# Kernel tuning notes

Hardware: AMD Instinct MI355X
Metric: run time of the kernel (lower is better)

Reference implementation:

```python
import jax, jax.numpy as jnp
import numpy as np

PC_RANGE = (-50.0, -50.0, -4.0, 50.0, 50.0, 4.0)
IMG_H, IMG_W = 256.0, 704.0
EPS = 1e-5


def _bilinear_sample(feat, u, v):
    # feat [H,W,C]; u,v [M] in [0,1]; matches F.grid_sample(align_corners=False, padding_mode='zeros')
    H, W, _ = feat.shape
    x = u * W - 0.5
    y = v * H - 0.5
    x0 = jnp.floor(x)
    y0 = jnp.floor(y)
    dx = (x - x0)[:, None]
    dy = (y - y0)[:, None]
    x0 = x0.astype(jnp.int32)
    y0 = y0.astype(jnp.int32)

    def g(xi, yi):
        inb = ((xi >= 0) & (xi < W) & (yi >= 0) & (yi < H)).astype(feat.dtype)[:, None]
        return feat[jnp.clip(yi, 0, H - 1), jnp.clip(xi, 0, W - 1)] * inb

    return (g(x0, y0) * (1 - dx) * (1 - dy) + g(x0 + 1, y0) * dx * (1 - dy)
            + g(x0, y0 + 1) * (1 - dx) * dy + g(x0 + 1, y0 + 1) * dx * dy)


def _conv1x1(t, w, b):
    return jnp.einsum('bchw,oc->bohw', t, w) + b[None, :, None, None]


def _inorm(t, eps=1e-5):
    # InstanceNorm2d (affine=False): normalize per (b, c) over spatial dims
    m = t.mean(axis=(2, 3), keepdims=True)
    var = t.var(axis=(2, 3), keepdims=True)
    return (t - m) * jax.lax.rsqrt(var + eps)


def _forward(feat, lidar2img, bev_pos, pe_w1, pe_b1, pe_w2, pe_b2, pe_w3, pe_b3,
             c1_w, c1_b, c2_w, c2_b, c3_w, c3_b):
    B, N, C, Hf, Wf = feat.shape
    _, P, Hb, Wb, _ = bev_pos.shape
    Q = Hb * Wb
    lo = jnp.asarray(PC_RANGE[:3], feat.dtype)
    hi = jnp.asarray(PC_RANGE[3:], feat.dtype)
    # 'b p h w d -> b (h w) p d', then scale normalized coords into pc_range
    ref01 = jnp.transpose(bev_pos, (0, 2, 3, 1, 4)).reshape(B, Q, P, 3)
    ref = ref01 * (hi - lo) + lo
    # project through per-camera lidar2img (homogeneous)
    pts = jnp.concatenate([ref, jnp.ones_like(ref[..., :1])], axis=-1)  # [B,Q,P,4]
    cam = jnp.einsum('bnij,bqpj->bnqpi', lidar2img, pts)                # [B,N,Q,P,4]
    homo = cam[..., 2]
    z = jnp.maximum(homo, EPS)
    u = cam[..., 0] / z / IMG_W
    v = cam[..., 1] / z / IMG_H
    valid = ((homo > EPS) & (u > 0.0) & (u < 1.0) & (v > 0.0) & (v < 1.0)).astype(feat.dtype)
    # bilinear gather per camera; feats to channel-last ('b n (g c) h w -> (b g) n h w c', G=1)
    fmap = jnp.transpose(feat, (0, 1, 3, 4, 2)).reshape(B * N, Hf, Wf, C)
    samp = jax.vmap(_bilinear_sample)(fmap, u.reshape(B * N, Q * P), v.reshape(B * N, Q * P))
    samp = samp.reshape(B, N, Q, P, C) * valid[..., None]
    samp = samp.sum(axis=1)  # sum over cameras -> [B,Q,P,C]
    # PositionalEncodingMap(3 -> 256 -> 256 -> 128) on normalized reference points
    pe = jax.nn.relu(ref01 @ pe_w1 + pe_b1)
    pe = jax.nn.relu(pe @ pe_w2 + pe_b2)
    pe = pe @ pe_w3 + pe_b3
    samp = samp + pe
    # 'b (h w) g p c -> b (p g c) h w' with g=1
    x = jnp.transpose(samp.reshape(B, Hb, Wb, P, C), (0, 3, 4, 1, 2)).reshape(B, P * C, Hb, Wb)
    gelu = lambda t: jax.nn.gelu(t, approximate=False)
    x = gelu(_inorm(_conv1x1(x, c1_w, c1_b)))
    x = gelu(_inorm(_conv1x1(x, c2_w, c2_b)))
    x = _conv1x1(x, c3_w, c3_b)
    return x


def setup_inputs() -> dict:
    key = jax.random.key(0)
    ks = jax.random.split(key, 16)
    B, N, C, Hf, Wf = 1, 6, 128, 32, 88
    P, Hb, Wb = 4, 160, 160
    E = 128
    MID = 256
    s = 0.02
    return {
        'feat': jax.random.normal(ks[0], (B, N, C, Hf, Wf), jnp.float32),
        'lidar2img': jax.random.normal(ks[1], (B, N, 4, 4), jnp.float32),
        'bev_pos': jax.random.uniform(ks[2], (B, P, Hb, Wb, 3), jnp.float32),
        'pe_w1': jax.random.normal(ks[3], (3, MID), jnp.float32) * s,
        'pe_b1': jnp.zeros((MID,), jnp.float32),
        'pe_w2': jax.random.normal(ks[4], (MID, MID), jnp.float32) * s,
        'pe_b2': jnp.zeros((MID,), jnp.float32),
        'pe_w3': jax.random.normal(ks[5], (MID, E), jnp.float32) * s,
        'pe_b3': jnp.zeros((E,), jnp.float32),
        'c1_w': jax.random.normal(ks[6], (4 * E, P * 128), jnp.float32) * s,
        'c1_b': jnp.zeros((4 * E,), jnp.float32),
        'c2_w': jax.random.normal(ks[7], (E, 4 * E), jnp.float32) * s,
        'c2_b': jnp.zeros((E,), jnp.float32),
        'c3_w': jax.random.normal(ks[8], (E, E), jnp.float32) * s,
        'c3_b': jnp.zeros((E,), jnp.float32),
    }


def reference(feat, lidar2img, bev_pos, pe_w1, pe_b1, pe_w2, pe_b2, pe_w3, pe_b3,
              c1_w, c1_b, c2_w, c2_b, c3_w, c3_b):
    return _forward(feat, lidar2img, bev_pos, pe_w1, pe_b1, pe_w2, pe_b2, pe_w3, pe_b3,
                    c1_w, c1_b, c2_w, c2_b, c3_w, c3_b)
```

## Files before the change

### kernel.cpp

```cpp
#include <hip/hip_runtime.h>
#include <cstdint>
#include <cstddef>

using frag8 = __attribute__((ext_vector_type(8))) short;
using f32x4 = __attribute__((ext_vector_type(4))) float;

__device__ __forceinline__ float b2f_bits(unsigned short u) {
    union { uint32_t u32; float f; } x; x.u32 = ((uint32_t)u) << 16; return x.f;
}
__device__ __forceinline__ float b2f_lo(uint32_t pk) {
    return __builtin_bit_cast(float, pk << 16);
}
__device__ __forceinline__ float b2f_hi(uint32_t pk) {
    return __builtin_bit_cast(float, pk & 0xffff0000u);
}
__device__ __forceinline__ unsigned short f2b(float f) {
    uint32_t u = __builtin_bit_cast(uint32_t, f);
    uint32_t r = (u + 0x7fffu + ((u >> 16) & 1u)) >> 16;
    return (unsigned short)r;
}

#define HF 32
#define WFEAT 88
#define NCAM 6
#define NPT 102400
#define BM 128
#define BN 128
#define BK 64

__global__ __launch_bounds__(256) void k_prep(const float* __restrict__ feat,
                                              const float* __restrict__ pw2,
                                              const float* __restrict__ pw3,
                                              const float* __restrict__ c1w,
                                              const float* __restrict__ c2w,
                                              const float* __restrict__ c3w,
                                              const float* __restrict__ l2i,
                                              const float* __restrict__ bev,
                                              unsigned short* __restrict__ featT,
                                              unsigned short* __restrict__ W2Tb,
                                              unsigned short* __restrict__ W3Tb,
                                              unsigned short* __restrict__ C1Wb,
                                              unsigned short* __restrict__ C2Wb,
                                              unsigned short* __restrict__ C3Wb,
                                              float* __restrict__ stats,
                                              int* __restrict__ poff,
                                              float4* __restrict__ pwts) {
    __shared__ unsigned short tile[64 * 132];
    int b = blockIdx.x, t = threadIdx.x;
    if (b < 2400) {
        int idx = b * 256 + t;
        int n = idx / NPT, pt = idx - n * NPT;
        int q = pt >> 2, p = pt & 3;
        int h = q / 160, w = q - h * 160;
        const float* bv = bev + ((p * 160 + h) * 160 + w) * 3;
        float rx = bv[0] * 100.f - 50.f;
        float ry = bv[1] * 100.f - 50.f;
        float rz = bv[2] * 8.f - 4.f;
        const float* M = l2i + n * 16;
        float c0   = M[0] * rx + M[1] * ry + M[2]  * rz + M[3];
        float c1v  = M[4] * rx + M[5] * ry + M[6]  * rz + M[7];
        float homo = M[8] * rx + M[9] * ry + M[10] * rz + M[11];
        float z = fmaxf(homo, 1e-5f);
        float u = c0 / z / 704.0f;
        float v = c1v / z / 256.0f;
        if (!(homo > 1e-5f && u > 0.f && u < 1.f && v > 0.f && v < 1.f)) {
            poff[idx] = -1;
            return;
        }
        float fx = u * (float)WFEAT - 0.5f;
        float fy = v * (float)HF - 0.5f;
        float fx0 = floorf(fx), fy0 = floorf(fy);
        float dx = fx - fx0, dy = fy - fy0;
        int x0 = (int)fx0, y0 = (int)fy0;
        float wxa = (x0 < 0) ? dx : 1.f - dx;
        float wxb = (x0 >= 0 && x0 < WFEAT - 1) ? dx : 0.f;
        float wya = (y0 < 0) ? dy : 1.f - dy;
        float wyb = (y0 >= 0 && y0 < HF - 1) ? dy : 0.f;
        int bx = max(x0, 0), by = max(y0, 0);
        poff[idx] = ((n * HF + by) * WFEAT + bx) << 7;
        pwts[idx] = make_float4(wxa * wya, wxb * wya, wxa * wyb, wxb * wyb);
        return;
    }
    b -= 2400;
    if (b < 264) {
        int n = b / 44;
        int s0 = (b - n * 44) * 64;
        #pragma unroll
        for (int i = 0; i < 32; ++i) {
            int e = i * 256 + t;
            int c = e >> 6, sl = e & 63;
            tile[sl * 132 + c] = f2b(feat[(size_t)(n * 128 + c) * 2816 + s0 + sl]);
        }
        __syncthreads();
        #pragma unroll
        for (int j = 0; j < 8; ++j) {
            int flat = j * 1024 + t * 4;
            int sl = flat >> 7, c = flat & 127;
            ushort4 v = *(const ushort4*)(tile + sl * 132 + c);
            *(ushort4*)(featT + (size_t)(n * 2816 + s0 + sl) * 128 + c) = v;
        }
        return;
    }
    b -= 264;
    if (b < 256) {
        int idx = b * 256 + t;
        int r = idx >> 8, c = idx & 255;
        W2Tb[c * 256 + r] = f2b(pw2[idx]);
        return;
    }
    b -= 256;
    if (b < 128) {
        int idx = b * 256 + t;
        int r = idx >> 7, c = idx & 127;
        W3Tb[c * 256 + r] = f2b(pw3[idx]);
        return;
    }
    b -= 128;
    if (b < 1024) { int idx = b * 256 + t; C1Wb[idx] = f2b(c1w[idx]); return; }
    b -= 1024;
    if (b < 256)  { int idx = b * 256 + t; C2Wb[idx] = f2b(c2w[idx]); return; }
    b -= 256;
    if (b < 64)   { int idx = b * 256 + t; C3Wb[idx] = f2b(c3w[idx]); return; }
    #pragma unroll
    for (int j = 0; j < 10; ++j) stats[t * 10 + j] = 0.f;
}

__global__ __launch_bounds__(256) void k_sample2(const unsigned short* __restrict__ featT,
                                                 const int* __restrict__ poff,
                                                 const float4* __restrict__ pwts,
                                                 unsigned short* __restrict__ samp) {
    int pt = blockIdx.x * 4 + (threadIdx.x >> 6);
    int lane = threadIdx.x & 63;
    int c2 = lane * 2;
    int offs[NCAM];
    float4 ww[NCAM];
    #pragma unroll
    for (int n = 0; n < NCAM; ++n) offs[n] = poff[n * NPT + pt];
    #pragma unroll
    for (int n = 0; n < NCAM; ++n) ww[n] = pwts[n * NPT + pt];
    float acc0 = 0.f, acc1 = 0.f;
    #pragma unroll
    for (int n = 0; n < NCAM; ++n) {
        if (offs[n] >= 0) {
            const unsigned short* base = featT + offs[n] + c2;
            uint32_t p00 = *(const uint32_t*)(base);
            uint32_t p01 = *(const uint32_t*)(base + 128);
            uint32_t p10 = *(const uint32_t*)(base + WFEAT * 128);
            uint32_t p11 = *(const uint32_t*)(base + WFEAT * 128 + 128);
            float4 w = ww[n];
            acc0 += w.x * b2f_lo(p00) + w.y * b2f_lo(p01) + w.z * b2f_lo(p10) + w.w * b2f_lo(p11);
            acc1 += w.x * b2f_hi(p00) + w.y * b2f_hi(p01) + w.z * b2f_hi(p10) + w.w * b2f_hi(p11);
        }
    }
    uint32_t outpk = (uint32_t)f2b(acc0) | ((uint32_t)f2b(acc1) << 16);
    *(uint32_t*)(samp + (size_t)pt * 128 + c2) = outpk;
}

__device__ __forceinline__ void stage_tile(const unsigned short* __restrict__ g, int ld,
                                           unsigned short* lds, int wave, int lane) {
    #pragma unroll
    for (int j = 0; j < 4; ++j) {
        int idx = wave * 256 + j * 64 + lane;
        int r = idx >> 3;
        int cs = idx & 7;
        int cl = cs ^ (r & 7);
        __builtin_amdgcn_global_load_lds(
            (const __attribute__((address_space(1))) void*)(g + (size_t)r * ld + cl * 8),
            (__attribute__((address_space(3))) void*)(lds + wave * 2048 + j * 512),
            16, 0, 0);
    }
}

__device__ __forceinline__ frag8 frag_read(const unsigned short* lds, int row, int chunk) {
    return *(const frag8*)(lds + row * 64 + ((chunk ^ (row & 7)) << 3));
}

__device__ __forceinline__ void mma_tile(const unsigned short* As, const unsigned short* Bs,
                                         int wm, int wn, int lane, f32x4 (&acc)[4][4]) {
    int lm = lane & 15, lq = lane >> 4;
    #pragma unroll
    for (int kk = 0; kk < 2; ++kk) {
        frag8 a[4], b[4];
        #pragma unroll
        for (int t = 0; t < 4; ++t) a[t] = frag_read(As, wm * 64 + t * 16 + lm, kk * 4 + lq);
        #pragma unroll
        for (int t = 0; t < 4; ++t) b[t] = frag_read(Bs, wn * 64 + t * 16 + lm, kk * 4 + lq);
        #pragma unroll
        for (int tm = 0; tm < 4; ++tm)
            #pragma unroll
            for (int tn = 0; tn < 4; ++tn)
                acc[tm][tn] = __builtin_amdgcn_mfma_f32_16x16x32_bf16(a[tm], b[tn], acc[tm][tn], 0, 0, 0);
    }
}

__global__ __launch_bounds__(256) void k_pe12(const float* __restrict__ bev,
                                              const float* __restrict__ pw1,
                                              const float* __restrict__ pb1,
                                              const unsigned short* __restrict__ Bt,
                                              const float* __restrict__ bias,
                                              unsigned short* __restrict__ H2) {
    __shared__ unsigned short As[BM * BK], Bs[BN * BK];
    __shared__ __align__(16) float wls[4 * 256];
    __shared__ float bevs[3 * 128];
    int t = threadIdx.x, lane = t & 63, wave = t >> 6;
    int wm = wave >> 1, wn = wave & 1;
    int m0 = blockIdx.x * BM, n0 = blockIdx.y * BN;
    {
        int i = t * 4;
        int j = i >> 8, c = i & 255;
        float4 v = (j < 3) ? *(const float4*)(pw1 + j * 256 + c)
                           : *(const float4*)(pb1 + c);
        *(float4*)(wls + i) = v;
    }
    if (t < 128) {
        int m = m0 + t;
        int q = m >> 2, p = m & 3;
        int h = q / 160, w = q - h * 160;
        const float* bv = bev + ((size_t)((p * 160 + h) * 160 + w)) * 3;
        bevs[t] = bv[0]; bevs[128 + t] = bv[1]; bevs[256 + t] = bv[2];
    }
    __syncthreads();
    int r = t & 127;
    int c0 = (t >> 7) * 4;
    float x = bevs[r], y = bevs[128 + r], z = bevs[256 + r];
    f32x4 acc[4][4] = {};
    for (int kt = 0; kt < 4; ++kt) {
        stage_tile(Bt + (size_t)n0 * 256 + kt * BK, 256, Bs, wave, lane);
        #pragma unroll
        for (int j = 0; j < 4; ++j) {
            int cl = c0 + j;
            const float* wp = wls + kt * 64 + cl * 8;
            float4 a0l = *(const float4*)(wp),       a0h = *(const float4*)(wp + 4);
            float4 a1l = *(const float4*)(wp + 256), a1h = *(const float4*)(wp + 260);
            float4 a2l = *(const float4*)(wp + 512), a2h = *(const float4*)(wp + 516);
            float4 bbl = *(const float4*)(wp + 768), bbh = *(const float4*)(wp + 772);
            uint32_t q0 = (uint32_t)f2b(fmaxf(x * a0l.x + y * a1l.x + z * a2l.x + bbl.x, 0.f))
                        | ((uint32_t)f2b(fmaxf(x * a0l.y + y * a1l.y + z * a2l.y + bbl.y, 0.f)) << 16);
            uint32_t q1 = (uint32_t)f2b(fmaxf(x * a0l.z + y * a1l.z + z * a2l.z + bbl.z, 0.f))
                        | ((uint32_t)f2b(fmaxf(x * a0l.w + y * a1l.w + z * a2l.w + bbl.w, 0.f)) << 16);
            uint32_t q2 = (uint32_t)f2b(fmaxf(x * a0h.x + y * a1h.x + z * a2h.x + bbh.x, 0.f))
                        | ((uint32_t)f2b(fmaxf(x * a0h.y + y * a1h.y + z * a2h.y + bbh.y, 0.f)) << 16);
            uint32_t q3 = (uint32_t)f2b(fmaxf(x * a0h.z + y * a1h.z + z * a2h.z + bbh.z, 0.f))
                        | ((uint32_t)f2b(fmaxf(x * a0h.w + y * a1h.w + z * a2h.w + bbh.w, 0.f)) << 16);
            *(uint4*)(As + r * 64 + ((cl ^ (r & 7)) << 3)) = make_uint4(q0, q1, q2, q3);
        }
        __syncthreads();
        mma_tile(As, Bs, wm, wn, lane, acc);
        __syncthreads();
    }
    int lm = lane & 15, lq = lane >> 4;
    #pragma unroll
    for (int tn = 0; tn < 4; ++tn) {
        int n = n0 + wn * 64 + tn * 16 + lm;
        float bn = bias[n];
        #pragma unroll
        for (int tm = 0; tm < 4; ++tm) {
            int mb = m0 + wm * 64 + tm * 16 + lq * 4;
            #pragma unroll
            for (int rr = 0; rr < 4; ++rr)
                H2[(size_t)(mb + rr) * 256 + n] = f2b(fmaxf(acc[tm][tn][rr] + bn, 0.f));
        }
    }
}

__global__ __launch_bounds__(256) void k_gemm_pe3(const unsigned short* __restrict__ A,
                                                  const unsigned short* __restrict__ Bt,
                                                  const float* __restrict__ bias,
                                                  const unsigned short* __restrict__ samp,
                                                  unsigned short* __restrict__ X) {
    __shared__ unsigned short As[BM * BK], Bs[BN * BK];
    int lane = threadIdx.x & 63, wave = threadIdx.x >> 6;
    int wm = wave >> 1, wn = wave & 1;
    int m0 = blockIdx.x * BM;
    f32x4 acc[4][4] = {};
    for (int kt = 0; kt < 4; ++kt) {
        stage_tile(A + (size_t)m0 * 256 + kt * BK, 256, As, wave, lane);
        stage_tile(Bt + (size_t)kt * BK, 256, Bs, wave, lane);
        __syncthreads();
        mma_tile(As, Bs, wm, wn, lane, acc);
        __syncthreads();
    }
    int lm = lane & 15, lq = lane >> 4;
    #pragma unroll
    for (int tn = 0; tn < 4; ++tn) {
        int n = wn * 64 + tn * 16 + lm;
        float bn = bias[n];
        #pragma unroll
        for (int tm = 0; tm < 4; ++tm) {
            int mb = m0 + wm * 64 + tm * 16 + lq * 4;
            #pragma unroll
            for (int rr = 0; rr < 4; ++rr) {
                size_t off = (size_t)(mb + rr) * 128 + n;
                X[off] = f2b(acc[tm][tn][rr] + bn + b2f_bits(samp[off]));
            }
        }
    }
}

template <int K, bool STATS>
__global__ __launch_bounds__(256) void k_gemm_conv(const unsigned short* __restrict__ A,
                                                   const unsigned short* __restrict__ Bt,
                                                   const float* __restrict__ bias,
                                                   unsigned short* __restrict__ Y, int ldY,
                                                   float* __restrict__ st, int C) {
    __shared__ unsigned short As[BM * BK], Bs[BN * BK];
    int lane = threadIdx.x & 63, wave = threadIdx.x >> 6;
    int wm = wave >> 1, wn = wave & 1;
    int m0 = blockIdx.x * BM, n0 = blockIdx.y * BN;
    f32x4 acc[4][4] = {};
    for (int kt = 0; kt < K / BK; ++kt) {
        stage_tile(A + (size_t)m0 * K + kt * BK, K, As, wave, lane);
        stage_tile(Bt + (size_t)n0 * K + kt * BK, K, Bs, wave, lane);
        __syncthreads();
        mma_tile(As, Bs, wm, wn, lane, acc);
        __syncthreads();
    }
    int lm = lane & 15, lq = lane >> 4;
    #pragma unroll
    for (int tn = 0; tn < 4; ++tn) {
        int n = n0 + wn * 64 + tn * 16 + lm;
        float bn = bias[n];
        float s1 = 0.f, s2 = 0.f;
        #pragma unroll
        for (int tm = 0; tm < 4; ++tm) {
            int mb = m0 + wm * 64 + tm * 16 + lq * 4;
            #pragma unroll
            for (int rr = 0; rr < 4; ++rr) {
                float v = acc[tm][tn][rr] + bn;
                Y[(size_t)(mb + rr) * ldY + n] = f2b(v);
                if (STATS) { s1 += v; s2 += v * v; }
            }
        }
        if (STATS) {
            s1 += __shfl_xor(s1, 16); s1 += __shfl_xor(s1, 32);
            s2 += __shfl_xor(s2, 16); s2 += __shfl_xor(s2, 32);
            if (lq == 0) { atomicAdd(&st[n], s1); atomicAdd(&st[C + n], s2); }
        }
    }
}

__global__ __launch_bounds__(256) void k_gemm_conv3(const unsigned short* __restrict__ A,
                                                    const unsigned short* __restrict__ Bt,
                                                    const float* __restrict__ bias,
                                                    float* __restrict__ out) {
    __shared__ unsigned short As[BM * BK], Bs[BN * BK];
    int lane = threadIdx.x & 63, wave = threadIdx.x >> 6;
    int wm = wave >> 1, wn = wave & 1;
    int m0 = blockIdx.x * BM;
    f32x4 acc[4][4] = {};
    for (int kt = 0; kt < 2; ++kt) {
        stage_tile(A + (size_t)m0 * 128 + kt * BK, 128, As, wave, lane);
        stage_tile(Bt + (size_t)kt * BK, 128, Bs, wave, lane);
        __syncthreads();
        mma_tile(As, Bs, wm, wn, lane, acc);
        __syncthreads();
    }
    int lm = lane & 15, lq = lane >> 4;
    #pragma unroll
    for (int tn = 0; tn < 4; ++tn) {
        int n = wn * 64 + tn * 16 + lm;
        float bn = bias[n];
        #pragma unroll
        for (int tm = 0; tm < 4; ++tm) {
            int mb = m0 + wm * 64 + tm * 16 + lq * 4;
            float4 pk;
            pk.x = acc[tm][tn][0] + bn;
            pk.y = acc[tm][tn][1] + bn;
            pk.z = acc[tm][tn][2] + bn;
            pk.w = acc[tm][tn][3] + bn;
            *(float4*)(out + (size_t)n * 25600 + mb) = pk;
        }
    }
}

__global__ void k_normgelu8f(const unsigned short* __restrict__ Y, const float* __restrict__ st,
                             unsigned short* __restrict__ X2, int Cmask, int C, float inv_n,
                             int total8) {
    int i8 = blockIdx.x * 256 + threadIdx.x;
    if (i8 >= total8) return;
    int e0 = i8 * 8;
    int c = e0 & Cmask;
    uint4 y = *(const uint4*)(Y + e0);
    float4 s1a = *(const float4*)(st + c);
    float4 s1b = *(const float4*)(st + c + 4);
    float4 s2a = *(const float4*)(st + C + c);
    float4 s2b = *(const float4*)(st + C + c + 4);
    float mu[8] = { s1a.x * inv_n, s1a.y * inv_n, s1a.z * inv_n, s1a.w * inv_n,
                    s1b.x * inv_n, s1b.y * inv_n, s1b.z * inv_n, s1b.w * inv_n };
    float sq[8] = { s2a.x, s2a.y, s2a.z, s2a.w, s2b.x, s2b.y, s2b.z, s2b.w };
    float rs[8];
    #pragma unroll
    for (int j = 0; j < 8; ++j) rs[j] = rsqrtf(sq[j] * inv_n - mu[j] * mu[j] + 1e-5f);
    const float is2 = 0.70710678118654752f;
    unsigned int yw[4] = {y.x, y.y, y.z, y.w};
    unsigned int ow[4];
    #pragma unroll
    for (int j = 0; j < 4; ++j) {
        float v0 = (b2f_bits((unsigned short)(yw[j] & 0xffffu)) - mu[j * 2]) * rs[j * 2];
        float v1 = (b2f_bits((unsigned short)(yw[j] >> 16)) - mu[j * 2 + 1]) * rs[j * 2 + 1];
        float g0 = 0.5f * v0 * (1.f + erff(v0 * is2));
        float g1 = 0.5f * v1 * (1.f + erff(v1 * is2));
        ow[j] = (uint32_t)f2b(g0) | ((uint32_t)f2b(g1) << 16);
    }
    *(uint4*)(X2 + e0) = make_uint4(ow[0], ow[1], ow[2], ow[3]);
}

extern "C" void kernel_launch(void* const* d_in, const int* in_sizes, int n_in,
                              void* d_out, int out_size, void* d_ws, size_t ws_size,
                              hipStream_t stream) {
    (void)in_sizes; (void)n_in; (void)out_size; (void)ws_size;
    const float* feat = (const float*)d_in[0];
    const float* l2i  = (const float*)d_in[1];
    const float* bev  = (const float*)d_in[2];
    const float* pw1  = (const float*)d_in[3];
    const float* pb1  = (const float*)d_in[4];
    const float* pw2  = (const float*)d_in[5];
    const float* pb2  = (const float*)d_in[6];
    const float* pw3  = (const float*)d_in[7];
    const float* pb3  = (const float*)d_in[8];
    const float* c1w  = (const float*)d_in[9];
    const float* c1b  = (const float*)d_in[10];
    const float* c2w  = (const float*)d_in[11];
    const float* c2b  = (const float*)d_in[12];
    const float* c3w  = (const float*)d_in[13];
    const float* c3b  = (const float*)d_in[14];
    float* outp = (float*)d_out;
    char* ws = (char*)d_ws;

    unsigned short* featT = (unsigned short*)(ws + 0);
    unsigned short* W2Tb  = (unsigned short*)(ws + 4348416);
    unsigned short* W3Tb  = (unsigned short*)(ws + 4479488);
    unsigned short* C1Wb  = (unsigned short*)(ws + 4545024);
    unsigned short* C2Wb  = (unsigned short*)(ws + 5069312);
    unsigned short* C3Wb  = (unsigned short*)(ws + 5200384);
    float* stats          = (float*)(ws + 5233152);
    int*    poff          = (int*)(ws + 5247488);
    float4* pwts          = (float4*)(ws + 7705088);
    char* BUF1 = ws + 17535488;
    char* BUF2 = ws + 69964288;
    char* BUF3 = ws + 122393088;

    float* st512 = stats;
    float* st128 = stats + 2048;

    unsigned short* H2   = (unsigned short*)BUF2;
    unsigned short* samp = (unsigned short*)BUF3;
    unsigned short* X    = (unsigned short*)BUF1;
    unsigned short* Y1   = (unsigned short*)BUF2;
    unsigned short* X2   = (unsigned short*)BUF3;
    unsigned short* Y2   = (unsigned short*)BUF1;
    unsigned short* X3   = (unsigned short*)(BUF1 + 6553600);

    k_prep<<<4393, 256, 0, stream>>>(feat, pw2, pw3, c1w, c2w, c3w, l2i, bev,
                                     featT, W2Tb, W3Tb, C1Wb, C2Wb, C3Wb, stats,
                                     poff, pwts);

    k_sample2<<<25600, 256, 0, stream>>>(featT, poff, pwts, samp);

    k_pe12<<<dim3(800, 2), 256, 0, stream>>>(bev, pw1, pb1, W2Tb, pb2, H2);
    k_gemm_pe3<<<dim3(800, 1), 256, 0, stream>>>(H2, W3Tb, pb3, samp, X);

    k_gemm_conv<512, true><<<dim3(200, 4), 256, 0, stream>>>(X, C1Wb, c1b, Y1, 512, st512, 512);
    k_normgelu8f<<<6400, 256, 0, stream>>>(Y1, st512, X2, 511, 512, 1.f / 25600.f, 1638400);

    k_gemm_conv<512, true><<<dim3(200, 1), 256, 0, stream>>>(X2, C2Wb, c2b, Y2, 128, st128, 128);
    k_normgelu8f<<<1600, 256, 0, stream>>>(Y2, st128, X3, 127, 128, 1.f / 25600.f, 409600);

    k_gemm_conv3<<<dim3(200, 1), 256, 0, stream>>>(X3, C3Wb, c3b, outp);
}
```

Before: 278.5 us.

## Fuse instance-norm+GELU into following GEMM prologues and double-buffer LDS tiles

Removes the two standalone norm+GELU kernels and applies normalization and GELU while loading A tiles inside the conv2 and conv3 GEMMs, so the normalized intermediates are never written to or read back from global memory. All GEMM kernels switch to double-buffered LDS so the next tile is staged while MFMAs run on the current one. The on-the-fly first PE layer in k_pe12 is overlapped the same way and now packs to bf16 with v_cvt_pk_bf16_f32. In exchange, LDS per block doubles, which may lower occupancy, and the erf work is repeated per block (conv2/conv3 have a single N tile, so nothing is recomputed).

```diff
diff --git a/kernel.cpp b/kernel.cpp
--- a/kernel.cpp
+++ b/kernel.cpp
@@ -18,6 +18,11 @@
     uint32_t u = __builtin_bit_cast(uint32_t, f);
     uint32_t r = (u + 0x7fffu + ((u >> 16) & 1u)) >> 16;
     return (unsigned short)r;
+}
+__device__ __forceinline__ uint32_t cvtpk_bf16(float lo, float hi) {
+    uint32_t r;
+    asm("v_cvt_pk_bf16_f32 %0, %1, %2" : "=v"(r) : "v"(lo), "v"(hi));
+    return r;
 }
 
 #define HF 32
@@ -193,13 +198,59 @@
     }
 }
 
+template <int KT>
+__device__ __forceinline__ void gemm_loop_db(const unsigned short* __restrict__ A, int ldA,
+                                             const unsigned short* __restrict__ B, int ldB,
+                                             unsigned short (*As)[BM * BK],
+                                             unsigned short (*Bs)[BN * BK],
+                                             int wave, int lane, int wm, int wn,
+                                             f32x4 (&acc)[4][4]) {
+    stage_tile(A, ldA, As[0], wave, lane);
+    stage_tile(B, ldB, Bs[0], wave, lane);
+    __syncthreads();
+    #pragma unroll
+    for (int kt = 0; kt < KT; ++kt) {
+        int cur = kt & 1, nxt = cur ^ 1;
+        if (kt + 1 < KT) {
+            stage_tile(A + (kt + 1) * BK, ldA, As[nxt], wave, lane);
+            stage_tile(B + (kt + 1) * BK, ldB, Bs[nxt], wave, lane);
+        }
+        mma_tile(As[cur], Bs[cur], wm, wn, lane, acc);
+        __syncthreads();
+    }
+}
+
+__device__ __forceinline__ void build_h1(const float* __restrict__ wls, float x, float y, float z,
+                                         int r, int c0, int kt, unsigned short* __restrict__ As) {
+    #pragma unroll
+    for (int j = 0; j < 4; ++j) {
+        int cl = c0 + j;
+        const float* wp = wls + kt * 64 + cl * 8;
+        float4 a0l = *(const float4*)(wp),       a0h = *(const float4*)(wp + 4);
+        float4 a1l = *(const float4*)(wp + 256), a1h = *(const float4*)(wp + 260);
+        float4 a2l = *(const float4*)(wp + 512), a2h = *(const float4*)(wp + 516);
+        float4 bbl = *(const float4*)(wp + 768), bbh = *(const float4*)(wp + 772);
+        float v0 = fmaxf(x * a0l.x + y * a1l.x + z * a2l.x + bbl.x, 0.f);
+        float v1 = fmaxf(x * a0l.y + y * a1l.y + z * a2l.y + bbl.y, 0.f);
+        float v2 = fmaxf(x * a0l.z + y * a1l.z + z * a2l.z + bbl.z, 0.f);
+        float v3 = fmaxf(x * a0l.w + y * a1l.w + z * a2l.w + bbl.w, 0.f);
+        float v4 = fmaxf(x * a0h.x + y * a1h.x + z * a2h.x + bbh.x, 0.f);
+        float v5 = fmaxf(x * a0h.y + y * a1h.y + z * a2h.y + bbh.y, 0.f);
+        float v6 = fmaxf(x * a0h.z + y * a1h.z + z * a2h.z + bbh.z, 0.f);
+        float v7 = fmaxf(x * a0h.w + y * a1h.w + z * a2h.w + bbh.w, 0.f);
+        uint32_t q0 = cvtpk_bf16(v0, v1), q1 = cvtpk_bf16(v2, v3);
+        uint32_t q2 = cvtpk_bf16(v4, v5), q3 = cvtpk_bf16(v6, v7);
+        *(uint4*)(As + r * 64 + ((cl ^ (r & 7)) << 3)) = make_uint4(q0, q1, q2, q3);
+    }
+}
+
 __global__ __launch_bounds__(256) void k_pe12(const float* __restrict__ bev,
                                               const float* __restrict__ pw1,
                                               const float* __restrict__ pb1,
                                               const unsigned short* __restrict__ Bt,
                                               const float* __restrict__ bias,
                                               unsigned short* __restrict__ H2) {
-    __shared__ unsigned short As[BM * BK], Bs[BN * BK];
+    __shared__ unsigned short As[2][BM * BK], Bs[2][BN * BK];
     __shared__ __align__(16) float wls[4 * 256];
     __shared__ float bevs[3 * 128];
     int t = threadIdx.x, lane = t & 63, wave = t >> 6;
@@ -224,28 +275,17 @@
     int c0 = (t >> 7) * 4;
     float x = bevs[r], y = bevs[128 + r], z = bevs[256 + r];
     f32x4 acc[4][4] = {};
+    stage_tile(Bt + (size_t)n0 * 256, 256, Bs[0], wave, lane);
+    build_h1(wls, x, y, z, r, c0, 0, As[0]);
+    __syncthreads();
+    #pragma unroll
     for (int kt = 0; kt < 4; ++kt) {
-        stage_tile(Bt + (size_t)n0 * 256 + kt * BK, 256, Bs, wave, lane);
-        #pragma unroll
-        for (int j = 0; j < 4; ++j) {
-            int cl = c0 + j;
-            const float* wp = wls + kt * 64 + cl * 8;
-            float4 a0l = *(const float4*)(wp),       a0h = *(const float4*)(wp + 4);
-            float4 a1l = *(const float4*)(wp + 256), a1h = *(const float4*)(wp + 260);
-            float4 a2l = *(const float4*)(wp + 512), a2h = *(const float4*)(wp + 516);
-            float4 bbl = *(const float4*)(wp + 768), bbh = *(const float4*)(wp + 772);
-            uint32_t q0 = (uint32_t)f2b(fmaxf(x * a0l.x + y * a1l.x + z * a2l.x + bbl.x, 0.f))
-                        | ((uint32_t)f2b(fmaxf(x * a0l.y + y * a1l.y + z * a2l.y + bbl.y, 0.f)) << 16);
-            uint32_t q1 = (uint32_t)f2b(fmaxf(x * a0l.z + y * a1l.z + z * a2l.z + bbl.z, 0.f))
-                        | ((uint32_t)f2b(fmaxf(x * a0l.w + y * a1l.w + z * a2l.w + bbl.w, 0.f)) << 16);
-            uint32_t q2 = (uint32_t)f2b(fmaxf(x * a0h.x + y * a1h.x + z * a2h.x + bbh.x, 0.f))
-                        | ((uint32_t)f2b(fmaxf(x * a0h.y + y * a1h.y + z * a2h.y + bbh.y, 0.f)) << 16);
-            uint32_t q3 = (uint32_t)f2b(fmaxf(x * a0h.z + y * a1h.z + z * a2h.z + bbh.z, 0.f))
-                        | ((uint32_t)f2b(fmaxf(x * a0h.w + y * a1h.w + z * a2h.w + bbh.w, 0.f)) << 16);
-            *(uint4*)(As + r * 64 + ((cl ^ (r & 7)) << 3)) = make_uint4(q0, q1, q2, q3);
-        }
-        __syncthreads();
-        mma_tile(As, Bs, wm, wn, lane, acc);
+        int cur = kt & 1, nxt = cur ^ 1;
+        if (kt < 3)
+            stage_tile(Bt + (size_t)n0 * 256 + (kt + 1) * BK, 256, Bs[nxt], wave, lane);
+        mma_tile(As[cur], Bs[cur], wm, wn, lane, acc);
+        if (kt < 3)
+            build_h1(wls, x, y, z, r, c0, kt + 1, As[nxt]);
         __syncthreads();
     }
     int lm = lane & 15, lq = lane >> 4;
@@ -268,18 +308,12 @@
                                                   const float* __restrict__ bias,
                                                   const unsigned short* __restrict__ samp,
                                                   unsigned short* __restrict__ X) {
-    __shared__ unsigned short As[BM * BK], Bs[BN * BK];
+    __shared__ unsigned short As[2][BM * BK], Bs[2][BN * BK];
     int lane = threadIdx.x & 63, wave = threadIdx.x >> 6;
     int wm = wave >> 1, wn = wave & 1;
     int m0 = blockIdx.x * BM;
     f32x4 acc[4][4] = {};
-    for (int kt = 0; kt < 4; ++kt) {
-        stage_tile(A + (size_t)m0 * 256 + kt * BK, 256, As, wave, lane);
-        stage_tile(Bt + (size_t)kt * BK, 256, Bs, wave, lane);
-        __syncthreads();
-        mma_tile(As, Bs, wm, wn, lane, acc);
-        __syncthreads();
-    }
+    gemm_loop_db<4>(A + (size_t)m0 * 256, 256, Bt, 256, As, Bs, wave, lane, wm, wn, acc);
     int lm = lane & 15, lq = lane >> 4;
     #pragma unroll
     for (int tn = 0; tn < 4; ++tn) {
@@ -303,18 +337,13 @@
                                                    const float* __restrict__ bias,
                                                    unsigned short* __restrict__ Y, int ldY,
                                                    float* __restrict__ st, int C) {
-    __shared__ unsigned short As[BM * BK], Bs[BN * BK];
+    __shared__ unsigned short As[2][BM * BK], Bs[2][BN * BK];
     int lane = threadIdx.x & 63, wave = threadIdx.x >> 6;
     int wm = wave >> 1, wn = wave & 1;
     int m0 = blockIdx.x * BM, n0 = blockIdx.y * BN;
     f32x4 acc[4][4] = {};
-    for (int kt = 0; kt < K / BK; ++kt) {
-        stage_tile(A + (size_t)m0 * K + kt * BK, K, As, wave, lane);
-        stage_tile(Bt + (size_t)n0 * K + kt * BK, K, Bs, wave, lane);
-        __syncthreads();
-        mma_tile(As, Bs, wm, wn, lane, acc);
-        __syncthreads();
-    }
+    gemm_loop_db<K / BK>(A + (size_t)m0 * K, K, Bt + (size_t)n0 * K, K,
+                         As, Bs, wave, lane, wm, wn, acc);
     int lm = lane & 15, lq = lane >> 4;
     #pragma unroll
     for (int tn = 0; tn < 4; ++tn) {
@@ -339,20 +368,125 @@
     }
 }
 
-__global__ __launch_bounds__(256) void k_gemm_conv3(const unsigned short* __restrict__ A,
-                                                    const unsigned short* __restrict__ Bt,
-                                                    const float* __restrict__ bias,
-                                                    float* __restrict__ out) {
-    __shared__ unsigned short As[BM * BK], Bs[BN * BK];
-    int lane = threadIdx.x & 63, wave = threadIdx.x >> 6;
+__device__ __forceinline__ void ng_load(const unsigned short* __restrict__ Ain, int ldA,
+                                        int m0, int k0, uint4 (&yv)[4], int wave, int lane) {
+    #pragma unroll
+    for (int j = 0; j < 4; ++j) {
+        int idx = wave * 256 + j * 64 + lane;
+        int r = idx >> 3, cs = idx & 7;
+        int cl = cs ^ (r & 7);
+        yv[j] = *(const uint4*)(Ain + (size_t)(m0 + r) * ldA + k0 + cl * 8);
+    }
+}
+
+__device__ __forceinline__ void ng_write(const uint4 (&yv)[4], const float* __restrict__ st,
+                                         int C, float inv_n, int k0,
+                                         unsigned short* __restrict__ lds, int wave, int lane) {
+    const float is2 = 0.70710678118654752f;
+    #pragma unroll
+    for (int j = 0; j < 4; ++j) {
+        int idx = wave * 256 + j * 64 + lane;
+        int r = idx >> 3, cs = idx & 7;
+        int cl = cs ^ (r & 7);
+        int k = k0 + cl * 8;
+        float4 s1a = *(const float4*)(st + k);
+        float4 s1b = *(const float4*)(st + k + 4);
+        float4 s2a = *(const float4*)(st + C + k);
+        float4 s2b = *(const float4*)(st + C + k + 4);
+        float s1[8] = {s1a.x, s1a.y, s1a.z, s1a.w, s1b.x, s1b.y, s1b.z, s1b.w};
+        float s2[8] = {s2a.x, s2a.y, s2a.z, s2a.w, s2b.x, s2b.y, s2b.z, s2b.w};
+        uint32_t yw[4] = {yv[j].x, yv[j].y, yv[j].z, yv[j].w};
+        uint32_t ow[4];
+        #pragma unroll
+        for (int i = 0; i < 4; ++i) {
+            float mu0 = s1[2 * i] * inv_n,     mu1 = s1[2 * i + 1] * inv_n;
+            float rs0 = rsqrtf(s2[2 * i] * inv_n - mu0 * mu0 + 1e-5f);
+            float rs1 = rsqrtf(s2[2 * i + 1] * inv_n - mu1 * mu1 + 1e-5f);
+            float v0 = (b2f_lo(yw[i]) - mu0) * rs0;
+            float v1 = (b2f_hi(yw[i]) - mu1) * rs1;
+            float g0 = 0.5f * v0 * (1.f + erff(v0 * is2));
+            float g1 = 0.5f * v1 * (1.f + erff(v1 * is2));
+            ow[i] = (uint32_t)f2b(g0) | ((uint32_t)f2b(g1) << 16);
+        }
+        *(uint4*)(lds + idx * 8) = make_uint4(ow[0], ow[1], ow[2], ow[3]);
+    }
+}
+
+__global__ __launch_bounds__(256) void k_gemm_conv2f(const unsigned short* __restrict__ Y1,
+                                                     const float* __restrict__ stIn,
+                                                     const unsigned short* __restrict__ Bt,
+                                                     const float* __restrict__ bias,
+                                                     unsigned short* __restrict__ Y2,
+                                                     float* __restrict__ stOut) {
+    __shared__ unsigned short As[2][BM * BK], Bs[2][BN * BK];
+    int t = threadIdx.x, lane = t & 63, wave = t >> 6;
     int wm = wave >> 1, wn = wave & 1;
     int m0 = blockIdx.x * BM;
+    const float inv_n = 1.f / 25600.f;
     f32x4 acc[4][4] = {};
+    uint4 yv[4];
+    ng_load(Y1, 512, m0, 0, yv, wave, lane);
+    stage_tile(Bt, 512, Bs[0], wave, lane);
+    ng_write(yv, stIn, 512, inv_n, 0, As[0], wave, lane);
+    __syncthreads();
+    #pragma unroll
+    for (int kt = 0; kt < 8; ++kt) {
+        int cur = kt & 1, nxt = cur ^ 1;
+        if (kt < 7) {
+            stage_tile(Bt + (kt + 1) * BK, 512, Bs[nxt], wave, lane);
+            ng_load(Y1, 512, m0, (kt + 1) * BK, yv, wave, lane);
+        }
+        mma_tile(As[cur], Bs[cur], wm, wn, lane, acc);
+        if (kt < 7) ng_write(yv, stIn, 512, inv_n, (kt + 1) * BK, As[nxt], wave, lane);
+        __syncthreads();
+    }
+    int lm = lane & 15, lq = lane >> 4;
+    #pragma unroll
+    for (int tn = 0; tn < 4; ++tn) {
+        int n = wn * 64 + tn * 16 + lm;
+        float bn = bias[n];
+        float s1 = 0.f, s2 = 0.f;
+        #pragma unroll
+        for (int tm = 0; tm < 4; ++tm) {
+            int mb = m0 + wm * 64 + tm * 16 + lq * 4;
+            #pragma unroll
+            for (int rr = 0; rr < 4; ++rr) {
+                float v = acc[tm][tn][rr] + bn;
+                Y2[(size_t)(mb + rr) * 128 + n] = f2b(v);
+                s1 += v; s2 += v * v;
+            }
+        }
+        s1 += __shfl_xor(s1, 16); s1 += __shfl_xor(s1, 32);
+        s2 += __shfl_xor(s2, 16); s2 += __shfl_xor(s2, 32);
+        if (lq == 0) { atomicAdd(&stOut[n], s1); atomicAdd(&stOut[128 + n], s2); }
+    }
+}
+
+__global__ __launch_bounds__(256) void k_gemm_conv3f(const unsigned short* __restrict__ Y2,
+                                                     const float* __restrict__ stIn,
+                                                     const unsigned short* __restrict__ Bt,
+                                                     const float* __restrict__ bias,
+                                                     float* __restrict__ out) {
+    __shared__ unsigned short As[2][BM * BK], Bs[2][BN * BK];
+    int t = threadIdx.x, lane = t & 63, wave = t >> 6;
+    int wm = wave >> 1, wn = wave & 1;
+    int m0 = blockIdx.x * BM;
+    const float inv_n = 1.f / 25600.f;
+    f32x4 acc[4][4] = {};
+    uint4 yv[4];
+    ng_load(Y2, 128, m0, 0, yv, wave, lane);
+    stage_tile(Bt, 128, Bs[0], wave, lane);
+    ng_write(yv, stIn, 128, inv_n, 0, As[0], wave, lane);
+    __syncthreads();
+    #pragma unroll
     for (int kt = 0; kt < 2; ++kt) {
-        stage_tile(A + (size_t)m0 * 128 + kt * BK, 128, As, wave, lane);
-        stage_tile(Bt + (size_t)kt * BK, 128, Bs, wave, lane);
-        __syncthreads();
-        mma_tile(As, Bs, wm, wn, lane, acc);
+        int cur = kt & 1, nxt = cur ^ 1;
+        if (kt < 1) {
+            stage_tile(Bt + (kt + 1) * BK, 128, Bs[nxt], wave, lane);
+            ng_load(Y2, 128, m0, (kt + 1) * BK, yv, wave, lane);
+        }
+        mma_tile(As[cur], Bs[cur], wm, wn, lane, acc);
+        if (kt < 1) ng_write(yv, stIn, 128, inv_n, (kt + 1) * BK, As[nxt], wave, lane);
         __syncthreads();
     }
     int lm = lane & 15, lq = lane >> 4;
@@ -371,38 +505,6 @@
             *(float4*)(out + (size_t)n * 25600 + mb) = pk;
         }
     }
-}
-
-__global__ void k_normgelu8f(const unsigned short* __restrict__ Y, const float* __restrict__ st,
-                             unsigned short* __restrict__ X2, int Cmask, int C, float inv_n,
-                             int total8) {
-    int i8 = blockIdx.x * 256 + threadIdx.x;
-    if (i8 >= total8) return;
-    int e0 = i8 * 8;
-    int c = e0 & Cmask;
-    uint4 y = *(const uint4*)(Y + e0);
-    float4 s1a = *(const float4*)(st + c);
-    float4 s1b = *(const float4*)(st + c + 4);
-    float4 s2a = *(const float4*)(st + C + c);
-    float4 s2b = *(const float4*)(st + C + c + 4);
-    float mu[8] = { s1a.x * inv_n, s1a.y * inv_n, s1a.z * inv_n, s1a.w * inv_n,
-                    s1b.x * inv_n, s1b.y * inv_n, s1b.z * inv_n, s1b.w * inv_n };
-    float sq[8] = { s2a.x, s2a.y, s2a.z, s2a.w, s2b.x, s2b.y, s2b.z, s2b.w };
-    float rs[8];
-    #pragma unroll
-    for (int j = 0; j < 8; ++j) rs[j] = rsqrtf(sq[j] * inv_n - mu[j] * mu[j] + 1e-5f);
-    const float is2 = 0.70710678118654752f;
-    unsigned int yw[4] = {y.x, y.y, y.z, y.w};
-    unsigned int ow[4];
-    #pragma unroll
-    for (int j = 0; j < 4; ++j) {
-        float v0 = (b2f_bits((unsigned short)(yw[j] & 0xffffu)) - mu[j * 2]) * rs[j * 2];
-        float v1 = (b2f_bits((unsigned short)(yw[j] >> 16)) - mu[j * 2 + 1]) * rs[j * 2 + 1];
-        float g0 = 0.5f * v0 * (1.f + erff(v0 * is2));
-        float g1 = 0.5f * v1 * (1.f + erff(v1 * is2));
-        ow[j] = (uint32_t)f2b(g0) | ((uint32_t)f2b(g1) << 16);
-    }
-    *(uint4*)(X2 + e0) = make_uint4(ow[0], ow[1], ow[2], ow[3]);
 }
 
 extern "C" void kernel_launch(void* const* d_in, const int* in_sizes, int n_in,
@@ -447,9 +549,7 @@
     unsigned short* samp = (unsigned short*)BUF3;
     unsigned short* X    = (unsigned short*)BUF1;
     unsigned short* Y1   = (unsigned short*)BUF2;
-    unsigned short* X2   = (unsigned short*)BUF3;
     unsigned short* Y2   = (unsigned short*)BUF1;
-    unsigned short* X3   = (unsigned short*)(BUF1 + 6553600);
 
     k_prep<<<4393, 256, 0, stream>>>(feat, pw2, pw3, c1w, c2w, c3w, l2i, bev,
                                      featT, W2Tb, W3Tb, C1Wb, C2Wb, C3Wb, stats,
@@ -461,10 +561,8 @@
     k_gemm_pe3<<<dim3(800, 1), 256, 0, stream>>>(H2, W3Tb, pb3, samp, X);
 
     k_gemm_conv<512, true><<<dim3(200, 4), 256, 0, stream>>>(X, C1Wb, c1b, Y1, 512, st512, 512);
-    k_normgelu8f<<<6400, 256, 0, stream>>>(Y1, st512, X2, 511, 512, 1.f / 25600.f, 1638400);
-
-    k_gemm_conv<512, true><<<dim3(200, 1), 256, 0, stream>>>(X2, C2Wb, c2b, Y2, 128, st128, 128);
-    k_normgelu8f<<<1600, 256, 0, stream>>>(Y2, st128, X3, 127, 128, 1.f / 25600.f, 409600);
-
-    k_gemm_conv3<<<dim3(200, 1), 256, 0, stream>>>(X3, C3Wb, c3b, outp);
-}
+
+    k_gemm_conv2f<<<dim3(200, 1), 256, 0, stream>>>(Y1, st512, C2Wb, c2b, Y2, st128);
+
+    k_gemm_conv3f<<<dim3(200, 1), 256, 0, stream>>>(Y2, st128, C3Wb, c3b, outp);
+}
```

Result: slower. 306.6 us (+10.1%).

## Fuse positional-encoding MLP layers into one kernel and double-buffer conv GEMMs

Applied to the files above, without the earlier changes.

Merges the pe layer1/2 kernel and the pe3 GEMM into a single kernel. Each block computes the full 256-wide hidden layer in registers, keeps H2 in shared memory, and runs the third layer with W3 fragments loaded straight from global. This removes the H2 global round trip and one launch, and stops layer 1 being recomputed for two N-tiles. The conv GEMMs get a double-buffered shared-memory K loop that overlaps staging of the next tile with MFMA. A hardware packed bf16 convert replaces the manual rounding for H1. The costs are higher register pressure (a 4x8 accumulator array), 64KB of shared memory per block that may limit occupancy, and uncached global reads of W3 per wave.

```diff
diff --git a/kernel.cpp b/kernel.cpp
--- a/kernel.cpp
+++ b/kernel.cpp
@@ -18,6 +18,11 @@
     uint32_t u = __builtin_bit_cast(uint32_t, f);
     uint32_t r = (u + 0x7fffu + ((u >> 16) & 1u)) >> 16;
     return (unsigned short)r;
+}
+__device__ __forceinline__ uint32_t cvtpk_bf16(float lo, float hi) {
+    uint32_t r;
+    asm("v_cvt_pk_bf16_f32 %0, %1, %2" : "=v"(r) : "v"(lo), "v"(hi));
+    return r;
 }
 
 #define HF 32
@@ -193,18 +198,71 @@
     }
 }
 
-__global__ __launch_bounds__(256) void k_pe12(const float* __restrict__ bev,
-                                              const float* __restrict__ pw1,
-                                              const float* __restrict__ pb1,
-                                              const unsigned short* __restrict__ Bt,
-                                              const float* __restrict__ bias,
-                                              unsigned short* __restrict__ H2) {
-    __shared__ unsigned short As[BM * BK], Bs[BN * BK];
-    __shared__ __align__(16) float wls[4 * 256];
-    __shared__ float bevs[3 * 128];
+template <int KT>
+__device__ __forceinline__ void gemm_loop_db(const unsigned short* __restrict__ A, int ldA,
+                                             const unsigned short* __restrict__ B, int ldB,
+                                             unsigned short (*As)[BM * BK],
+                                             unsigned short (*Bs)[BN * BK],
+                                             int wave, int lane, int wm, int wn,
+                                             f32x4 (&acc)[4][4]) {
+    stage_tile(A, ldA, As[0], wave, lane);
+    stage_tile(B, ldB, Bs[0], wave, lane);
+    __syncthreads();
+    #pragma unroll
+    for (int kt = 0; kt < KT; ++kt) {
+        int cur = kt & 1, nxt = cur ^ 1;
+        if (kt + 1 < KT) {
+            stage_tile(A + (kt + 1) * BK, ldA, As[nxt], wave, lane);
+            stage_tile(B + (kt + 1) * BK, ldB, Bs[nxt], wave, lane);
+        }
+        mma_tile(As[cur], Bs[cur], wm, wn, lane, acc);
+        __syncthreads();
+    }
+}
+
+__device__ __forceinline__ void build_h1(const float* __restrict__ wls, float x, float y, float z,
+                                         int r, int c0, int kt, unsigned short* __restrict__ As) {
+    #pragma unroll
+    for (int j = 0; j < 4; ++j) {
+        int cl = c0 + j;
+        const float* wp = wls + kt * 64 + cl * 8;
+        float4 a0l = *(const float4*)(wp),       a0h = *(const float4*)(wp + 4);
+        float4 a1l = *(const float4*)(wp + 256), a1h = *(const float4*)(wp + 260);
+        float4 a2l = *(const float4*)(wp + 512), a2h = *(const float4*)(wp + 516);
+        float4 bbl = *(const float4*)(wp + 768), bbh = *(const float4*)(wp + 772);
+        float v0 = fmaxf(x * a0l.x + y * a1l.x + z * a2l.x + bbl.x, 0.f);
+        float v1 = fmaxf(x * a0l.y + y * a1l.y + z * a2l.y + bbl.y, 0.f);
+        float v2 = fmaxf(x * a0l.z + y * a1l.z + z * a2l.z + bbl.z, 0.f);
+        float v3 = fmaxf(x * a0l.w + y * a1l.w + z * a2l.w + bbl.w, 0.f);
+        float v4 = fmaxf(x * a0h.x + y * a1h.x + z * a2h.x + bbh.x, 0.f);
+        float v5 = fmaxf(x * a0h.y + y * a1h.y + z * a2h.y + bbh.y, 0.f);
+        float v6 = fmaxf(x * a0h.z + y * a1h.z + z * a2h.z + bbh.z, 0.f);
+        float v7 = fmaxf(x * a0h.w + y * a1h.w + z * a2h.w + bbh.w, 0.f);
+        uint32_t q0 = cvtpk_bf16(v0, v1), q1 = cvtpk_bf16(v2, v3);
+        uint32_t q2 = cvtpk_bf16(v4, v5), q3 = cvtpk_bf16(v6, v7);
+        *(uint4*)(As + r * 64 + ((cl ^ (r & 7)) << 3)) = make_uint4(q0, q1, q2, q3);
+    }
+}
+
+__global__ __launch_bounds__(256) void k_pe123(const float* __restrict__ bev,
+                                               const float* __restrict__ pw1,
+                                               const float* __restrict__ pb1,
+                                               const unsigned short* __restrict__ W2t,
+                                               const float* __restrict__ pb2,
+                                               const unsigned short* __restrict__ W3t,
+                                               const float* __restrict__ pb3,
+                                               const unsigned short* __restrict__ samp,
+                                               unsigned short* __restrict__ X) {
+    __shared__ __align__(16) char smem[65536];
+    unsigned short* As  = (unsigned short*)smem;
+    unsigned short* Bs  = (unsigned short*)(smem + 16384);
+    float* wls  = (float*)(smem + 49152);
+    float* bevs = (float*)(smem + 53248);
+    unsigned short* H2s = (unsigned short*)smem;
+
     int t = threadIdx.x, lane = t & 63, wave = t >> 6;
     int wm = wave >> 1, wn = wave & 1;
-    int m0 = blockIdx.x * BM, n0 = blockIdx.y * BN;
+    int m0 = blockIdx.x * BM;
     {
         int i = t * 4;
         int j = i >> 8, c = i & 255;
@@ -223,75 +281,84 @@
     int r = t & 127;
     int c0 = (t >> 7) * 4;
     float x = bevs[r], y = bevs[128 + r], z = bevs[256 + r];
-    f32x4 acc[4][4] = {};
+    int lm = lane & 15, lq = lane >> 4;
+
+    f32x4 acc[4][8] = {};
     for (int kt = 0; kt < 4; ++kt) {
-        stage_tile(Bt + (size_t)n0 * 256 + kt * BK, 256, Bs, wave, lane);
-        #pragma unroll
-        for (int j = 0; j < 4; ++j) {
-            int cl = c0 + j;
-            const float* wp = wls + kt * 64 + cl * 8;
-            float4 a0l = *(const float4*)(wp),       a0h = *(const float4*)(wp + 4);
-            float4 a1l = *(const float4*)(wp + 256), a1h = *(const float4*)(wp + 260);
-            float4 a2l = *(const float4*)(wp + 512), a2h = *(const float4*)(wp + 516);
-            float4 bbl = *(const float4*)(wp + 768), bbh = *(const float4*)(wp + 772);
-            uint32_t q0 = (uint32_t)f2b(fmaxf(x * a0l.x + y * a1l.x + z * a2l.x + bbl.x, 0.f))
-                        | ((uint32_t)f2b(fmaxf(x * a0l.y + y * a1l.y + z * a2l.y + bbl.y, 0.f)) << 16);
-            uint32_t q1 = (uint32_t)f2b(fmaxf(x * a0l.z + y * a1l.z + z * a2l.z + bbl.z, 0.f))
-                        | ((uint32_t)f2b(fmaxf(x * a0l.w + y * a1l.w + z * a2l.w + bbl.w, 0.f)) << 16);
-            uint32_t q2 = (uint32_t)f2b(fmaxf(x * a0h.x + y * a1h.x + z * a2h.x + bbh.x, 0.f))
-                        | ((uint32_t)f2b(fmaxf(x * a0h.y + y * a1h.y + z * a2h.y + bbh.y, 0.f)) << 16);
-            uint32_t q3 = (uint32_t)f2b(fmaxf(x * a0h.z + y * a1h.z + z * a2h.z + bbh.z, 0.f))
-                        | ((uint32_t)f2b(fmaxf(x * a0h.w + y * a1h.w + z * a2h.w + bbh.w, 0.f)) << 16);
-            *(uint4*)(As + r * 64 + ((cl ^ (r & 7)) << 3)) = make_uint4(q0, q1, q2, q3);
-        }
+        stage_tile(W2t + kt * BK, 256, Bs, wave, lane);
+        stage_tile(W2t + 128 * 256 + kt * BK, 256, Bs + 8192, wave, lane);
+        build_h1(wls, x, y, z, r, c0, kt, As);
         __syncthreads();
-        mma_tile(As, Bs, wm, wn, lane, acc);
+        #pragma unroll
+        for (int kk = 0; kk < 2; ++kk) {
+            int ch = kk * 4 + lq;
+            frag8 a[4], b[8];
+            #pragma unroll
+            for (int tt = 0; tt < 4; ++tt) a[tt] = frag_read(As, wm * 64 + tt * 16 + lm, ch);
+            #pragma unroll
+            for (int tn = 0; tn < 8; ++tn) {
+                int brow = (tn < 4 ? wn * 64 + tn * 16 : 128 + wn * 64 + (tn - 4) * 16) + lm;
+                b[tn] = frag_read(Bs, brow, ch);
+            }
+            #pragma unroll
+            for (int tm = 0; tm < 4; ++tm)
+                #pragma unroll
+                for (int tn = 0; tn < 8; ++tn)
+                    acc[tm][tn] = __builtin_amdgcn_mfma_f32_16x16x32_bf16(a[tm], b[tn], acc[tm][tn], 0, 0, 0);
+        }
         __syncthreads();
     }
-    int lm = lane & 15, lq = lane >> 4;
+
+    #pragma unroll
+    for (int tn = 0; tn < 8; ++tn) {
+        int n = (tn < 4 ? wn * 64 + tn * 16 : 128 + wn * 64 + (tn - 4) * 16) + lm;
+        float bn = pb2[n];
+        int kt2 = n >> 6, chs = (n >> 3) & 7, e = n & 7;
+        #pragma unroll
+        for (int tm = 0; tm < 4; ++tm) {
+            int rb = wm * 64 + tm * 16 + lq * 4;
+            #pragma unroll
+            for (int rr = 0; rr < 4; ++rr) {
+                int row = rb + rr;
+                H2s[kt2 * 8192 + row * 64 + ((chs ^ (row & 7)) << 3) + e] =
+                    f2b(fmaxf(acc[tm][tn][rr] + bn, 0.f));
+            }
+        }
+    }
+    __syncthreads();
+
+    f32x4 acc2[4][4] = {};
+    #pragma unroll
+    for (int kt = 0; kt < 4; ++kt) {
+        #pragma unroll
+        for (int kk = 0; kk < 2; ++kk) {
+            int ch = kk * 4 + lq;
+            frag8 a[4], b[4];
+            #pragma unroll
+            for (int tt = 0; tt < 4; ++tt)
+                a[tt] = frag_read(H2s + kt * 8192, wm * 64 + tt * 16 + lm, ch);
+            #pragma unroll
+            for (int tn = 0; tn < 4; ++tn)
+                b[tn] = *(const frag8*)(W3t + (size_t)(wn * 64 + tn * 16 + lm) * 256 + kt * 64 + ch * 8);
+            #pragma unroll
+            for (int tm = 0; tm < 4; ++tm)
+                #pragma unroll
+                for (int tn = 0; tn < 4; ++tn)
+                    acc2[tm][tn] = __builtin_amdgcn_mfma_f32_16x16x32_bf16(a[tm], b[tn], acc2[tm][tn], 0, 0, 0);
+        }
+    }
+
     #pragma unroll
     for (int tn = 0; tn < 4; ++tn) {
-        int n = n0 + wn * 64 + tn * 16 + lm;
-        float bn = bias[n];
+        int n = wn * 64 + tn * 16 + lm;
+        float bn = pb3[n];
         #pragma unroll
         for (int tm = 0; tm < 4; ++tm) {
             int mb = m0 + wm * 64 + tm * 16 + lq * 4;
             #pragma unroll
-            for (int rr = 0; rr < 4; ++rr)
-                H2[(size_t)(mb + rr) * 256 + n] = f2b(fmaxf(acc[tm][tn][rr] + bn, 0.f));
-        }
-    }
-}
-
-__global__ __launch_bounds__(256) void k_gemm_pe3(const unsigned short* __restrict__ A,
-                                                  const unsigned short* __restrict__ Bt,
-                                                  const float* __restrict__ bias,
-                                                  const unsigned short* __restrict__ samp,
-                                                  unsigned short* __restrict__ X) {
-    __shared__ unsigned short As[BM * BK], Bs[BN * BK];
-    int lane = threadIdx.x & 63, wave = threadIdx.x >> 6;
-    int wm = wave >> 1, wn = wave & 1;
-    int m0 = blockIdx.x * BM;
-    f32x4 acc[4][4] = {};
-    for (int kt = 0; kt < 4; ++kt) {
-        stage_tile(A + (size_t)m0 * 256 + kt * BK, 256, As, wave, lane);
-        stage_tile(Bt + (size_t)kt * BK, 256, Bs, wave, lane);
-        __syncthreads();
-        mma_tile(As, Bs, wm, wn, lane, acc);
-        __syncthreads();
-    }
-    int lm = lane & 15, lq = lane >> 4;
-    #pragma unroll
-    for (int tn = 0; tn < 4; ++tn) {
-        int n = wn * 64 + tn * 16 + lm;
-        float bn = bias[n];
-        #pragma unroll
-        for (int tm = 0; tm < 4; ++tm) {
-            int mb = m0 + wm * 64 + tm * 16 + lq * 4;
-            #pragma unroll
             for (int rr = 0; rr < 4; ++rr) {
                 size_t off = (size_t)(mb + rr) * 128 + n;
-                X[off] = f2b(acc[tm][tn][rr] + bn + b2f_bits(samp[off]));
+                X[off] = f2b(acc2[tm][tn][rr] + bn + b2f_bits(samp[off]));
             }
         }
     }
@@ -303,18 +370,13 @@
                                                    const float* __restrict__ bias,
                                                    unsigned short* __restrict__ Y, int ldY,
                                                    float* __restrict__ st, int C) {
-    __shared__ unsigned short As[BM * BK], Bs[BN * BK];
+    __shared__ unsigned short As[2][BM * BK], Bs[2][BN * BK];
     int lane = threadIdx.x & 63, wave = threadIdx.x >> 6;
     int wm = wave >> 1, wn = wave & 1;
     int m0 = blockIdx.x * BM, n0 = blockIdx.y * BN;
     f32x4 acc[4][4] = {};
-    for (int kt = 0; kt < K / BK; ++kt) {
-        stage_tile(A + (size_t)m0 * K + kt * BK, K, As, wave, lane);
-        stage_tile(Bt + (size_t)n0 * K + kt * BK, K, Bs, wave, lane);
-        __syncthreads();
-        mma_tile(As, Bs, wm, wn, lane, acc);
-        __syncthreads();
-    }
+    gemm_loop_db<K / BK>(A + (size_t)m0 * K, K, Bt + (size_t)n0 * K, K,
+                         As, Bs, wave, lane, wm, wn, acc);
     int lm = lane & 15, lq = lane >> 4;
     #pragma unroll
     for (int tn = 0; tn < 4; ++tn) {
@@ -343,18 +405,12 @@
                                                     const unsigned short* __restrict__ Bt,
                                                     const float* __restrict__ bias,
                                                     float* __restrict__ out) {
-    __shared__ unsigned short As[BM * BK], Bs[BN * BK];
+    __shared__ unsigned short As[2][BM * BK], Bs[2][BN * BK];
     int lane = threadIdx.x & 63, wave = threadIdx.x >> 6;
     int wm = wave >> 1, wn = wave & 1;
     int m0 = blockIdx.x * BM;
     f32x4 acc[4][4] = {};
-    for (int kt = 0; kt < 2; ++kt) {
-        stage_tile(A + (size_t)m0 * 128 + kt * BK, 128, As, wave, lane);
-        stage_tile(Bt + (size_t)kt * BK, 128, Bs, wave, lane);
-        __syncthreads();
-        mma_tile(As, Bs, wm, wn, lane, acc);
-        __syncthreads();
-    }
+    gemm_loop_db<2>(A + (size_t)m0 * 128, 128, Bt, 128, As, Bs, wave, lane, wm, wn, acc);
     int lm = lane & 15, lq = lane >> 4;
     #pragma unroll
     for (int tn = 0; tn < 4; ++tn) {
@@ -443,7 +499,6 @@
     float* st512 = stats;
     float* st128 = stats + 2048;
 
-    unsigned short* H2   = (unsigned short*)BUF2;
     unsigned short* samp = (unsigned short*)BUF3;
     unsigned short* X    = (unsigned short*)BUF1;
     unsigned short* Y1   = (unsigned short*)BUF2;
@@ -457,8 +512,7 @@
 
     k_sample2<<<25600, 256, 0, stream>>>(featT, poff, pwts, samp);
 
-    k_pe12<<<dim3(800, 2), 256, 0, stream>>>(bev, pw1, pb1, W2Tb, pb2, H2);
-    k_gemm_pe3<<<dim3(800, 1), 256, 0, stream>>>(H2, W3Tb, pb3, samp, X);
+    k_pe123<<<800, 256, 0, stream>>>(bev, pw1, pb1, W2Tb, pb2, W3Tb, pb3, samp, X);
 
     k_gemm_conv<512, true><<<dim3(200, 4), 256, 0, stream>>>(X, C1Wb, c1b, Y1, 512, st512, 512);
     k_normgelu8f<<<6400, 256, 0, stream>>>(Y1, st512, X2, 511, 512, 1.f / 25600.f, 1638400);
@@ -466,5 +520,5 @@
     k_gemm_conv<512, true><<<dim3(200, 1), 256, 0, stream>>>(X2, C2Wb, c2b, Y2, 128, st128, 128);
     k_normgelu8f<<<1600, 256, 0, stream>>>(Y2, st128, X3, 127, 128, 1.f / 25600.f, 409600);
 
-    k_gemm_conv3<<<dim3(200, 1), 256, 0, stream>>>(X3, C3Wb, c3b, outp);
-}
+    k_gemm_conv3<<<200, 256, 0, stream>>>(X3, C3Wb, c3b, outp);
+}
```

Result: slower. 319.3 us (+14.6%).
